# Kernel optimization log

Measured on AMD Instinct MI355X. Metric: run time of the kernel, lower is better.

Reference implementation:

```python
import jax, jax.numpy as jnp
import numpy as np

B, L, D, K, J = 8, 2048, 1024, 32, 512


def setup_inputs() -> dict:
    key = jax.random.key(0)
    ks = jax.random.split(key, 12)
    w = lambda k: jax.random.normal(k, (D, D), jnp.float32) * 0.02
    z = jnp.zeros((D,), jnp.float32)
    return {
        "seg0": jax.random.normal(ks[0], (B, L, D), jnp.float32),
        "seg1": jax.random.normal(ks[1], (B, L, D), jnp.float32),
        "prompt_embed": jax.random.normal(ks[2], (1, 1, D), jnp.float32),
        "Wq_mem": w(ks[3]), "bq_mem": z,
        "Wk_mem": w(ks[4]), "bk_mem": z,
        "Wq": w(ks[5]), "bq": z,
        "Wk": w(ks[6]), "bk": z,
        "Wv": w(ks[7]), "bv": z,
        "Wo": w(ks[8]), "bo": z,
    }


def reference(seg0, seg1, prompt_embed, Wq_mem, bq_mem, Wk_mem, bk_mem,
              Wq, bq, Wk, bk, Wv, bv, Wo, bo):
    scale = 1.0 / np.sqrt(D).astype(np.float32)  # n_heads=1 so d_k = d_model

    def backbone(X):  # single-head SDPA, X: [B, S, D]
        Q = X @ Wq + bq
        Kh = X @ Wk + bk
        V = X @ Wv + bv
        scores = jnp.einsum('bqd,bkd->bqk', Q, Kh) * scale
        attn = jax.nn.softmax(scores, axis=-1)
        out = jnp.einsum('bqk,bkd->bqd', attn, V)
        return out @ Wo + bo

    def summarize(H):  # -> [B, 1, D]
        T = jnp.broadcast_to(prompt_embed, (H.shape[0], 1, D))
        inp = jnp.concatenate([T, H[:, :J, :], T], axis=1)  # [B, J+2, D]
        return backbone(inp)[:, J:J + 1, :]

    # ---- segment 1: memory bank empty -> retrieval is zeros ----
    P0 = jnp.zeros((B, 1, D), seg0.dtype)
    input_h0 = jnp.concatenate([P0, seg0, P0], axis=1)  # [B, L+2, D]
    H_out0 = backbone(input_h0)[:, K + 1:L + K + 2, :]   # clamped slice -> [B, 2017, D]
    out0 = H_out0[:, :-1, :]                             # [B, 2016, D]
    M1 = H_out0[:, -1, :]                                # [B, D] stored memory
    prev_sensory = seg0[:, -K:, :]                       # [B, K, D]

    # ---- segment 2: soft retrieval over 1-entry memory bank ----
    S1 = summarize(seg1)                                 # [B, 1, D]
    M_past = M1[None]                                    # [1, B, D]
    Qn = S1 @ Wq_mem + bq_mem                            # [B, 1, D]
    Kp = M_past @ Wk_mem + bk_mem                        # [1, B, D]
    scores = jnp.matmul(Qn, jnp.swapaxes(Kp, -2, -1)) * scale  # [B, 1, B]
    attn = jax.nn.softmax(scores, axis=-1)
    P1 = jnp.matmul(attn, M_past)                        # [B, 1, D]

    input_h1 = jnp.concatenate([prev_sensory, P1, seg1, P1], axis=1)  # [B, K+L+2, D]
    H_out1 = backbone(input_h1)[:, K + 1:L + K + 2, :]   # [B, 2049, D]
    out1 = H_out1[:, :-1, :]                             # [B, 2048, D]
    return (out0, out1)
```

## Files before the change

kernel.cpp:

```cpp
#include <hip/hip_runtime.h>
#include <stdint.h>
#include <stddef.h>

#define DIM    1024
#define NBATCH 8
#define SEQL   2048
#define JSUM   512
#define SPMAX  2304
#define SPS    768

typedef unsigned long long ull;
typedef __attribute__((ext_vector_type(8))) __bf16 bf16x8;
typedef __attribute__((ext_vector_type(8))) short  short8;
typedef __attribute__((ext_vector_type(4))) float  floatx4;

__device__ __forceinline__ short f2bf(float f) {
  unsigned u = __builtin_bit_cast(unsigned, f);
  u = (u + 0x7fffu + ((u >> 16) & 1u)) >> 16;
  return (short)u;
}
__device__ __forceinline__ float bf2f(short s) {
  unsigned u = ((unsigned)(unsigned short)s) << 16;
  return __builtin_bit_cast(float, u);
}

__device__ __forceinline__ void glds16(const short* g, short8* l) {
  __builtin_amdgcn_global_load_lds(
      (const __attribute__((address_space(1))) unsigned int*)g,
      (__attribute__((address_space(3))) unsigned int*)l, 16, 0, 0);
}

#define VMCNT(n) do { asm volatile("s_waitcnt vmcnt(" #n ")" ::: "memory"); \
                      __builtin_amdgcn_sched_barrier(0); } while (0)

__device__ __forceinline__ void barrier_raw() {
  asm volatile("" ::: "memory");
  __builtin_amdgcn_s_barrier();
  asm volatile("" ::: "memory");
}

struct GemmP {
  const short* A; ull sA; int ldA;
  const short* B; ull sB; int ldB;
  short* C; ull sC;
  int N, Kd;
  const float* bias;
  float* dst0; int t_lo, t_hi, outT;
  float* dstSp; int t_sp, Spad;
  int gx;
  int nblk;
  int mode;
  int swiz;
};

__global__ __launch_bounds__(512, 2)
void gemm_nt(GemmP q0, GemmP q1)
{
  const int  pid = blockIdx.x;
  const bool s1  = pid >= q0.nblk;
  const GemmP& q = s1 ? q1 : q0;
  const int  lid = s1 ? (pid - q0.nblk) : pid;

  int tn, tm, bz;
  if (q.swiz == 1) {
    bz = lid & 7;
    const int s = lid >> 3;
    tn = s % q.gx;
    tm = s / q.gx;
  } else {
    tm = lid % q.gx;
    tn = lid / q.gx;
    bz = 0;
  }

  const short* A  = q.A + (ull)bz * q.sA;
  const short* Bm = q.B + (ull)bz * q.sB;

  const int tid  = threadIdx.x;
  const int wave = tid >> 6, lane = tid & 63;

  __shared__ short8 ldsA[2][2048];
  __shared__ short8 ldsB[2][2048];

  const int r0  = tid & 255;
  const int k80 = tid >> 8;
  const short* pA = A  + (long long)(tm * 256 + r0) * q.ldA + k80 * 8;
  const short* pB = Bm + (long long)(tn * 256 + r0) * q.ldB + k80 * 8;

  floatx4 acc[8][4];
#pragma unroll
  for (int i = 0; i < 8; i++)
#pragma unroll
    for (int j = 0; j < 4; j++) acc[i][j] = (floatx4)(0.0f);

  const int wm = (wave >> 2) * 128;
  const int wn = (wave & 3) * 64;
  const int fr = lane & 15;
  const int fq = lane >> 4;

  const int nt = q.Kd >> 6;

  glds16(pA,      &ldsA[0][tid]);
  glds16(pA + 16, &ldsA[0][tid + 512]);
  glds16(pB,      &ldsB[0][tid]);
  glds16(pB + 16, &ldsB[0][tid + 512]);
  glds16(pA + 32, &ldsA[0][1024 + tid]);
  glds16(pA + 48, &ldsA[0][1024 + tid + 512]);
  glds16(pB + 32, &ldsB[0][1024 + tid]);
  glds16(pB + 48, &ldsB[0][1024 + tid + 512]);
  VMCNT(4);
  barrier_raw();

  for (int t = 0; t < nt; t++) {
    const short8* LA = ldsA[t & 1];
    const short8* LB = ldsB[t & 1];
    const int  nb   = (t + 1) & 1;
    const int  koff = (t + 1) * 64;
    const bool stg  = (t + 1) < nt;

    bf16x8 af[4], bv[4];

    {
      const int ka = fq * 256;
#pragma unroll
      for (int n2 = 0; n2 < 4; n2++)
        bv[n2] = __builtin_bit_cast(bf16x8, LB[ka + wn + n2 * 16 + fr]);
#pragma unroll
      for (int mt = 0; mt < 4; mt++)
        af[mt] = __builtin_bit_cast(bf16x8, LA[ka + wm + mt * 16 + fr]);
      if (stg) {
        glds16(pA + koff,      &ldsA[nb][tid]);
        glds16(pA + koff + 16, &ldsA[nb][tid + 512]);
      }
      __builtin_amdgcn_s_setprio(1);
#pragma unroll
      for (int mt = 0; mt < 4; mt++)
#pragma unroll
        for (int n2 = 0; n2 < 4; n2++)
          acc[mt][n2] = __builtin_amdgcn_mfma_f32_16x16x32_bf16(
              af[mt], bv[n2], acc[mt][n2], 0, 0, 0);
      __builtin_amdgcn_s_setprio(0);
#pragma unroll
      for (int mt = 0; mt < 4; mt++)
        af[mt] = __builtin_bit_cast(bf16x8, LA[ka + wm + 64 + mt * 16 + fr]);
      if (stg) {
        glds16(pB + koff,      &ldsB[nb][tid]);
        glds16(pB + koff + 16, &ldsB[nb][tid + 512]);
      }
      __builtin_amdgcn_s_setprio(1);
#pragma unroll
      for (int mt = 0; mt < 4; mt++)
#pragma unroll
        for (int n2 = 0; n2 < 4; n2++)
          acc[4 + mt][n2] = __builtin_amdgcn_mfma_f32_16x16x32_bf16(
              af[mt], bv[n2], acc[4 + mt][n2], 0, 0, 0);
      __builtin_amdgcn_s_setprio(0);
      if (stg) VMCNT(4); else VMCNT(0);
      barrier_raw();
    }

    {
      const int ka = (fq + 4) * 256;
#pragma unroll
      for (int n2 = 0; n2 < 4; n2++)
        bv[n2] = __builtin_bit_cast(bf16x8, LB[ka + wn + n2 * 16 + fr]);
#pragma unroll
      for (int mt = 0; mt < 4; mt++)
        af[mt] = __builtin_bit_cast(bf16x8, LA[ka + wm + mt * 16 + fr]);
      if (stg) {
        glds16(pA + koff + 32, &ldsA[nb][1024 + tid]);
        glds16(pA + koff + 48, &ldsA[nb][1024 + tid + 512]);
      }
      __builtin_amdgcn_s_setprio(1);
#pragma unroll
      for (int mt = 0; mt < 4; mt++)
#pragma unroll
        for (int n2 = 0; n2 < 4; n2++)
          acc[mt][n2] = __builtin_amdgcn_mfma_f32_16x16x32_bf16(
              af[mt], bv[n2], acc[mt][n2], 0, 0, 0);
      __builtin_amdgcn_s_setprio(0);
#pragma unroll
      for (int mt = 0; mt < 4; mt++)
        af[mt] = __builtin_bit_cast(bf16x8, LA[ka + wm + 64 + mt * 16 + fr]);
      if (stg) {
        glds16(pB + koff + 32, &ldsB[nb][1024 + tid]);
        glds16(pB + koff + 48, &ldsB[nb][1024 + tid + 512]);
      }
      __builtin_amdgcn_s_setprio(1);
#pragma unroll
      for (int mt = 0; mt < 4; mt++)
#pragma unroll
        for (int n2 = 0; n2 < 4; n2++)
          acc[4 + mt][n2] = __builtin_amdgcn_mfma_f32_16x16x32_bf16(
              af[mt], bv[n2], acc[4 + mt][n2], 0, 0, 0);
      __builtin_amdgcn_s_setprio(0);
      if (stg) VMCNT(4);
      barrier_raw();
    }
  }

  if (q.mode == 3) {
    const int bb  = (tm * 256) / q.Spad;
    const int rb0 = tm * 256 - bb * q.Spad + wm + fq * 4;
#pragma unroll
    for (int mf = 0; mf < 8; mf++) {
#pragma unroll
      for (int n2 = 0; n2 < 4; n2++) {
        const int col = tn * 256 + wn + n2 * 16 + fr;
#pragma unroll
        for (int r = 0; r < 4; r++) {
          const int tt = rb0 + (mf >> 2) * 64 + (mf & 3) * 16 + r;
          float v = acc[mf][n2][r] + q.bias[col];
          if (tt >= q.t_lo && tt < q.t_hi)
            q.dst0[((size_t)bb * q.outT + (tt - q.t_lo)) * DIM + col] = v;
          else if (tt == q.t_sp)
            q.dstSp[(size_t)bb * DIM + col] = v;
        }
      }
    }
  } else {
    short* C = q.C + (ull)bz * q.sC;
#pragma unroll
    for (int mf = 0; mf < 8; mf++) {
#pragma unroll
      for (int n2 = 0; n2 < 4; n2++) {
        const int col = tn * 256 + wn + n2 * 16 + fr;
        float bn = (q.mode == 1) ? q.bias[col] : 0.0f;
#pragma unroll
        for (int r = 0; r < 4; r++) {
          const int row = tm * 256 + wm + (mf >> 2) * 64 + (mf & 3) * 16 + fq * 4 + r;
          float v = acc[mf][n2][r] + bn;
          if (q.mode == 2) v += q.bias[row];
          C[(size_t)row * q.N + col] = f2bf(v);
        }
      }
    }
  }
}

__global__ __launch_bounds__(256)
void softmax_rows2(short* __restrict__ SA0, int Spad0, int S0, int nx0,
                   short* __restrict__ SA1, int Spad1, int S1, float scale)
{
  __shared__ float buf[SPMAX];
  __shared__ float red[8];
  int t = blockIdx.x;
  const int b = blockIdx.y;
  short* row; int Spad, S;
  if (t < nx0) { row = SA0 + ((size_t)b * Spad0 + t) * Spad0; Spad = Spad0; S = S0; }
  else { t -= nx0; row = SA1 + ((size_t)b * Spad1 + t) * Spad1; Spad = Spad1; S = S1; }
  const int tid = threadIdx.x;
  const int nv = S >> 3;

  float mx = -1e30f;
  for (int g = tid; g < nv; g += 256) {
    short8 v = ((const short8*)row)[g];
#pragma unroll
    for (int j = 0; j < 8; j++) {
      float f = bf2f(v[j]) * scale;
      buf[g * 8 + j] = f;
      mx = fmaxf(mx, f);
    }
  }
  for (int i = (nv << 3) + tid; i < S; i += 256) {
    float f = bf2f(row[i]) * scale;
    buf[i] = f;
    mx = fmaxf(mx, f);
  }
  for (int off = 32; off; off >>= 1) mx = fmaxf(mx, __shfl_down(mx, off, 64));
  if ((tid & 63) == 0) red[tid >> 6] = mx;
  __syncthreads();
  if (tid == 0) {
    float m = red[0];
    for (int w = 1; w < 4; w++) m = fmaxf(m, red[w]);
    red[0] = m;
  }
  __syncthreads();
  mx = red[0];

  float sum = 0.f;
  for (int i = tid; i < S; i += 256) {
    float e = __expf(buf[i] - mx);
    buf[i] = e;
    sum += e;
  }
  for (int off = 32; off; off >>= 1) sum += __shfl_down(sum, off, 64);
  if ((tid & 63) == 0) red[4 + (tid >> 6)] = sum;
  __syncthreads();
  if (tid == 0) red[4] = 1.0f / (red[4] + red[5] + red[6] + red[7]);
  __syncthreads();
  const float rinv = red[4];

  for (int g = tid; g < nv; g += 256) {
    short8 o;
#pragma unroll
    for (int j = 0; j < 8; j++) o[j] = f2bf(buf[g * 8 + j] * rinv);
    ((short8*)row)[g] = o;
  }
  for (int i = (nv << 3) + tid; i < S; i += 256) row[i] = f2bf(buf[i] * rinv);
  for (int i = S + tid; i < Spad; i += 256) row[i] = 0;
}

__global__ __launch_bounds__(256)
void wtrans(const float* __restrict__ W, short* __restrict__ WT)
{
  __shared__ float tile[32][33];
  const int bn = blockIdx.x * 32, bk = blockIdx.y * 32;
  const int tx = threadIdx.x & 31, ty = threadIdx.x >> 5;
#pragma unroll
  for (int j = 0; j < 4; j++)
    tile[ty + j * 8][tx] = W[(size_t)(bk + ty + j * 8) * DIM + bn + tx];
  __syncthreads();
#pragma unroll
  for (int j = 0; j < 4; j++)
    WT[(size_t)(bn + ty + j * 8) * DIM + bk + tx] = f2bf(tile[tx][ty + j * 8]);
}

__global__ __launch_bounds__(256)
void bcat(const float* __restrict__ a, const float* __restrict__ b,
          float* __restrict__ o)
{
  const int i = blockIdx.x * 256 + threadIdx.x;
  o[i] = (i < DIM) ? a[i] : b[i - DIM];
}

__global__ __launch_bounds__(256)
void assemble0(const float* __restrict__ seg0, short* __restrict__ X)
{
  const int Spad = SPMAX;
  const int b = blockIdx.y;
  const size_t lin = ((size_t)blockIdx.x * 256 + threadIdx.x) * 4;
  const int t = (int)(lin >> 10), d = (int)(lin & 1023);
  float4 v = make_float4(0.f, 0.f, 0.f, 0.f);
  if (t >= 1 && t <= SEQL)
    v = *(const float4*)(seg0 + ((size_t)b * SEQL + (t - 1)) * DIM + d);
  union { short s[4]; ull u; } o;
  o.s[0] = f2bf(v.x); o.s[1] = f2bf(v.y); o.s[2] = f2bf(v.z); o.s[3] = f2bf(v.w);
  *(ull*)(X + (size_t)b * Spad * DIM + lin) = o.u;
}

__global__ __launch_bounds__(256)
void assembleS(const float* __restrict__ seg1, const float* __restrict__ prompt,
               short* __restrict__ X)
{
  const int Spad = SPS;
  const int b = blockIdx.y;
  const size_t lin = ((size_t)blockIdx.x * 256 + threadIdx.x) * 4;
  const int t = (int)(lin >> 10), d = (int)(lin & 1023);
  float4 v = make_float4(0.f, 0.f, 0.f, 0.f);
  if (t == 0 || t == JSUM + 1)
    v = *(const float4*)(prompt + d);
  else if (t >= 1 && t <= JSUM)
    v = *(const float4*)(seg1 + ((size_t)b * SEQL + (t - 1)) * DIM + d);
  union { short s[4]; ull u; } o;
  o.s[0] = f2bf(v.x); o.s[1] = f2bf(v.y); o.s[2] = f2bf(v.z); o.s[3] = f2bf(v.w);
  *(ull*)(X + (size_t)b * Spad * DIM + lin) = o.u;
}

__global__ __launch_bounds__(256)
void assemble1(const float* __restrict__ seg0, const float* __restrict__ seg1,
               const float* __restrict__ P1, short* __restrict__ X)
{
  const int Spad = SPMAX;
  const int b = blockIdx.y;
  const size_t lin = ((size_t)blockIdx.x * 256 + threadIdx.x) * 4;
  const int t = (int)(lin >> 10), d = (int)(lin & 1023);
  float4 v = make_float4(0.f, 0.f, 0.f, 0.f);
  if (t < 32)
    v = *(const float4*)(seg0 + ((size_t)b * SEQL + (SEQL - 32 + t)) * DIM + d);
  else if (t == 32 || t == 2081)
    v = *(const float4*)(P1 + (size_t)b * DIM + d);
  else if (t >= 33 && t <= 2080)
    v = *(const float4*)(seg1 + ((size_t)b * SEQL + (t - 33)) * DIM + d);
  union { short s[4]; ull u; } o;
  o.s[0] = f2bf(v.x); o.s[1] = f2bf(v.y); o.s[2] = f2bf(v.z); o.s[3] = f2bf(v.w);
  *(ull*)(X + (size_t)b * Spad * DIM + lin) = o.u;
}

__global__ __launch_bounds__(256)
void mem_proj(const float* __restrict__ Sb, const float* __restrict__ M1,
              const float* __restrict__ Wq_mem, const float* __restrict__ bq_mem,
              const float* __restrict__ Wk_mem, const float* __restrict__ bk_mem,
              float* __restrict__ Qn, float* __restrict__ Kp)
{
  const int n = blockIdx.x * 256 + threadIdx.x;
  const int b = blockIdx.y;
  const int w = blockIdx.z;
  const float* x    = w ? M1 : Sb;
  const float* W    = w ? Wk_mem : Wq_mem;
  const float* bias = w ? bk_mem : bq_mem;
  float* o          = w ? Kp : Qn;
  const float* xr = x + (size_t)b * DIM;
  float s = bias[n];
  for (int k = 0; k < DIM; k++) s += xr[k] * W[(size_t)k * DIM + n];
  o[(size_t)b * DIM + n] = s;
}

__global__ __launch_bounds__(256)
void mem_attn(const float* __restrict__ Qn, const float* __restrict__ Kp,
              const float* __restrict__ M1, float* __restrict__ P1, float scale)
{
  __shared__ float red[256];
  __shared__ float w8[8];
  const int b = blockIdx.x, tid = threadIdx.x;
  for (int bp = 0; bp < NBATCH; bp++) {
    float p = 0.f;
    for (int k = tid; k < DIM; k += 256)
      p += Qn[(size_t)b * DIM + k] * Kp[(size_t)bp * DIM + k];
    red[tid] = p; __syncthreads();
    for (int off = 128; off; off >>= 1) {
      if (tid < off) red[tid] += red[tid + off];
      __syncthreads();
    }
    if (tid == 0) w8[bp] = red[0] * scale;
    __syncthreads();
  }
  if (tid == 0) {
    float m = w8[0];
    for (int i = 1; i < NBATCH; i++) m = fmaxf(m, w8[i]);
    float s = 0.f;
    for (int i = 0; i < NBATCH; i++) { w8[i] = __expf(w8[i] - m); s += w8[i]; }
    for (int i = 0; i < NBATCH; i++) w8[i] /= s;
  }
  __syncthreads();
  for (int d = tid; d < DIM; d += 256) {
    float a = 0.f;
    for (int bp = 0; bp < NBATCH; bp++) a += w8[bp] * M1[(size_t)bp * DIM + d];
    P1[(size_t)b * DIM + d] = a;
  }
}

extern "C" void kernel_launch(void* const* d_in, const int* in_sizes, int n_in,
                              void* d_out, int out_size, void* d_ws, size_t ws_size,
                              hipStream_t stream)
{
  const float* seg0   = (const float*)d_in[0];
  const float* seg1   = (const float*)d_in[1];
  const float* prompt = (const float*)d_in[2];
  const float* Wq_mem = (const float*)d_in[3];
  const float* bq_mem = (const float*)d_in[4];
  const float* Wk_mem = (const float*)d_in[5];
  const float* bk_mem = (const float*)d_in[6];
  const float* Wq     = (const float*)d_in[7];
  const float* bq     = (const float*)d_in[8];
  const float* Wk     = (const float*)d_in[9];
  const float* bk     = (const float*)d_in[10];
  const float* Wv     = (const float*)d_in[11];
  const float* bv     = (const float*)d_in[12];
  const float* Wo     = (const float*)d_in[13];
  const float* bo     = (const float*)d_in[14];
  float* outp = (float*)d_out;

  const size_t WSZ   = (size_t)DIM * DIM * 2;
  const size_t XSZ   = (size_t)NBATCH * SPMAX * DIM * 2;
  const size_t SASZ  = (size_t)NBATCH * SPMAX * SPMAX * 2;
  const size_t XSZS  = (size_t)NBATCH * SPS * DIM * 2;
  const size_t SASZS = (size_t)NBATCH * SPS * SPS * 2;
  const size_t VSZ   = (size_t)NBATCH * DIM * 4;

  char* p = (char*)d_ws;
  short* WqT  = (short*)p; p += WSZ;
  short* WkT  = (short*)p; p += WSZ;
  short* WvT  = (short*)p; p += WSZ;
  short* WoT  = (short*)p; p += WSZ;
  short* X    = (short*)p; p += XSZ;
  short* QKb  = (short*)p; p += 2 * XSZ;
  short* Vt   = (short*)p; p += XSZ;
  short* Ctx  = (short*)p; p += XSZ;
  short* SA   = (short*)p; p += SASZ;
  short* XS   = (short*)p; p += XSZS;
  short* QKbS = (short*)p; p += 2 * XSZS;
  short* VtS  = (short*)p; p += XSZS;
  short* CtxS = (short*)p; p += XSZS;
  short* SAS  = (short*)p; p += SASZS;
  float* M1b  = (float*)p; p += VSZ;
  float* Sb   = (float*)p; p += VSZ;
  float* Qn   = (float*)p; p += VSZ;
  float* Kp   = (float*)p; p += VSZ;
  float* P1   = (float*)p; p += VSZ;
  float* bqk  = (float*)p; p += 2 * DIM * 4;

  const float scale = 0.03125f;
  dim3 blk(256, 1, 1);
  dim3 blkG(512, 1, 1);

  auto P = [](const short* A, ull sA, int ldA,
              const short* B, ull sB, int ldB,
              short* C, ull sC, int N, int Kd, const float* bias,
              float* dst0, int t_lo, int t_hi, int outT,
              float* dstSp, int t_sp, int Spad, int gx, int nblk,
              int mode, int swiz) {
    GemmP q{A, sA, ldA, B, sB, ldB, C, sC, N, Kd, bias,
            dst0, t_lo, t_hi, outT, dstSp, t_sp, Spad, gx, nblk, mode, swiz};
    return q;
  };

  wtrans<<<dim3(32, 32), blk, 0, stream>>>(Wq, WqT);
  wtrans<<<dim3(32, 32), blk, 0, stream>>>(Wk, WkT);
  wtrans<<<dim3(32, 32), blk, 0, stream>>>(Wv, WvT);
  wtrans<<<dim3(32, 32), blk, 0, stream>>>(Wo, WoT);
  bcat<<<dim3(8), blk, 0, stream>>>(bq, bk, bqk);

  assemble0<<<dim3(SPMAX, NBATCH), blk, 0, stream>>>(seg0, X);
  assembleS<<<dim3(SPS, NBATCH), blk, 0, stream>>>(seg1, prompt, XS);

  {
    GemmP a = P(X, 0, DIM, WqT, 0, DIM, QKb, 0, 2048, DIM, bqk,
                nullptr, 0, 0, 0, nullptr, -1, SPMAX, NBATCH * SPMAX / 256, 576, 1, 2);
    GemmP b = P(XS, 0, DIM, WqT, 0, DIM, QKbS, 0, 2048, DIM, bqk,
                nullptr, 0, 0, 0, nullptr, -1, SPS, NBATCH * SPS / 256, 192, 1, 2);
    gemm_nt<<<dim3(768), blkG, 0, stream>>>(a, b);
  }
  {
    GemmP a = P(WvT, 0, DIM, X, (ull)SPMAX * DIM, DIM,
                Vt, (ull)DIM * SPMAX, SPMAX, DIM, bv,
                nullptr, 0, 0, 0, nullptr, -1, SPMAX, SPMAX / 256, 288, 2, 1);
    GemmP b = P(WvT, 0, DIM, XS, (ull)SPS * DIM, DIM,
                VtS, (ull)DIM * SPS, SPS, DIM, bv,
                nullptr, 0, 0, 0, nullptr, -1, SPS, SPS / 256, 96, 2, 1);
    gemm_nt<<<dim3(384), blkG, 0, stream>>>(a, b);
  }
  {
    GemmP a = P(QKb, (ull)SPMAX * 2048, 2048, QKb + DIM, (ull)SPMAX * 2048, 2048,
                SA, (ull)SPMAX * SPMAX, SPMAX, DIM, nullptr,
                nullptr, 0, 0, 0, nullptr, -1, SPMAX, SPMAX / 256, 648, 0, 1);
    GemmP b = P(QKbS, (ull)SPS * 2048, 2048, QKbS + DIM, (ull)SPS * 2048, 2048,
                SAS, (ull)SPS * SPS, SPS, DIM, nullptr,
                nullptr, 0, 0, 0, nullptr, -1, SPS, SPS / 256, 72, 0, 1);
    gemm_nt<<<dim3(720), blkG, 0, stream>>>(a, b);
  }
  softmax_rows2<<<dim3(SPMAX + SPS, NBATCH), blk, 0, stream>>>(
      SA, SPMAX, 2050, SPMAX, SAS, SPS, 514, scale);
  {
    GemmP a = P(SA, (ull)SPMAX * SPMAX, SPMAX, Vt, (ull)DIM * SPMAX, SPMAX,
                Ctx, (ull)SPMAX * DIM, DIM, 2112, nullptr,
                nullptr, 0, 0, 0, nullptr, -1, SPMAX, DIM / 256, 288, 0, 1);
    GemmP b = P(SAS, (ull)SPS * SPS, SPS, VtS, (ull)DIM * SPS, SPS,
                CtxS, (ull)SPS * DIM, DIM, 576, nullptr,
                nullptr, 0, 0, 0, nullptr, -1, SPS, DIM / 256, 96, 0, 1);
    gemm_nt<<<dim3(384), blkG, 0, stream>>>(a, b);
  }
  {
    GemmP a = P(Ctx, 0, DIM, WoT, 0, DIM, nullptr, 0, DIM, DIM, bo,
                outp, 33, 2049, 2016, M1b, 2049, SPMAX, NBATCH * SPMAX / 256, 288, 3, 2);
    GemmP b = P(CtxS, 0, DIM, WoT, 0, DIM, nullptr, 0, DIM, DIM, bo,
                nullptr, 0, 0, 0, Sb, JSUM, SPS, NBATCH * SPS / 256, 96, 3, 2);
    gemm_nt<<<dim3(384), blkG, 0, stream>>>(a, b);
  }

  mem_proj<<<dim3(DIM / 256, NBATCH, 2), blk, 0, stream>>>(
      Sb, M1b, Wq_mem, bq_mem, Wk_mem, bk_mem, Qn, Kp);
  mem_attn<<<dim3(NBATCH), blk, 0, stream>>>(Qn, Kp, M1b, P1, scale);

  assemble1<<<dim3(SPMAX, NBATCH), blk, 0, stream>>>(seg0, seg1, P1, X);
  {
    GemmP a = P(X, 0, DIM, WqT, 0, DIM, QKb, 0, 2048, DIM, bqk,
                nullptr, 0, 0, 0, nullptr, -1, SPMAX, NBATCH * SPMAX / 256, 576, 1, 2);
    GemmP b = P(WvT, 0, DIM, X, (ull)SPMAX * DIM, DIM,
                Vt, (ull)DIM * SPMAX, SPMAX, DIM, bv,
                nullptr, 0, 0, 0, nullptr, -1, SPMAX, SPMAX / 256, 288, 2, 1);
    gemm_nt<<<dim3(864), blkG, 0, stream>>>(a, b);
  }
  {
    GemmP a = P(QKb, (ull)SPMAX * 2048, 2048, QKb + DIM, (ull)SPMAX * 2048, 2048,
                SA, (ull)SPMAX * SPMAX, SPMAX, DIM, nullptr,
                nullptr, 0, 0, 0, nullptr, -1, SPMAX, SPMAX / 256, 648, 0, 1);
    gemm_nt<<<dim3(648), blkG, 0, stream>>>(a, a);
  }
  softmax_rows2<<<dim3(SPMAX, NBATCH), blk, 0, stream>>>(
      SA, SPMAX, 2082, SPMAX, SA, SPMAX, 2082, scale);
  {
    GemmP a = P(SA, (ull)SPMAX * SPMAX, SPMAX, Vt, (ull)DIM * SPMAX, SPMAX,
                Ctx, (ull)SPMAX * DIM, DIM, 2112, nullptr,
                nullptr, 0, 0, 0, nullptr, -1, SPMAX, DIM / 256, 288, 0, 1);
    gemm_nt<<<dim3(288), blkG, 0, stream>>>(a, a);
  }
  {
    GemmP a = P(Ctx, 0, DIM, WoT, 0, DIM, nullptr, 0, DIM, DIM, bo,
                outp + (size_t)NBATCH * 2016 * DIM, 33, 2081, 2048,
                nullptr, -1, SPMAX, NBATCH * SPMAX / 256, 288, 3, 2);
    gemm_nt<<<dim3(288), blkG, 0, stream>>>(a, a);
  }
}
```

Baseline: 1.484 ms.

## Use 1024-thread GEMM blocks with 64x64 per-wave subtiles and unfuse QK/V launch

The bf16 GEMM block grows from 512 to 1024 threads (16 waves). Each wave now computes a 64x64 subtile instead of 128x64, halving accumulator registers, and each thread issues half as many global-to-LDS loads per stage. An extra barrier is added before each MFMA phase. The segment-2 fused QK-projection and V-transpose GEMM launch is split into two separate launches. The intent is more waves per CU for latency hiding, at the cost of lower per-wave arithmetic intensity, more LDS traffic per MFMA and extra synchronisation.

After: 1.990 ms. 1.34x slower.

```diff
diff --git a/kernel.cpp b/kernel.cpp
--- a/kernel.cpp
+++ b/kernel.cpp
@@ -53,7 +53,7 @@
   int swiz;
 };
 
-__global__ __launch_bounds__(512, 2)
+__global__ __launch_bounds__(1024)
 void gemm_nt(GemmP q0, GemmP q1)
 {
   const int  pid = blockIdx.x;
@@ -87,13 +87,13 @@
   const short* pA = A  + (long long)(tm * 256 + r0) * q.ldA + k80 * 8;
   const short* pB = Bm + (long long)(tn * 256 + r0) * q.ldB + k80 * 8;
 
-  floatx4 acc[8][4];
-#pragma unroll
-  for (int i = 0; i < 8; i++)
+  floatx4 acc[4][4];
+#pragma unroll
+  for (int i = 0; i < 4; i++)
 #pragma unroll
     for (int j = 0; j < 4; j++) acc[i][j] = (floatx4)(0.0f);
 
-  const int wm = (wave >> 2) * 128;
+  const int wm = (wave >> 2) * 64;
   const int wn = (wave & 3) * 64;
   const int fr = lane & 15;
   const int fq = lane >> 4;
@@ -101,14 +101,10 @@
   const int nt = q.Kd >> 6;
 
   glds16(pA,      &ldsA[0][tid]);
-  glds16(pA + 16, &ldsA[0][tid + 512]);
   glds16(pB,      &ldsB[0][tid]);
-  glds16(pB + 16, &ldsB[0][tid + 512]);
   glds16(pA + 32, &ldsA[0][1024 + tid]);
-  glds16(pA + 48, &ldsA[0][1024 + tid + 512]);
   glds16(pB + 32, &ldsB[0][1024 + tid]);
-  glds16(pB + 48, &ldsB[0][1024 + tid + 512]);
-  VMCNT(4);
+  VMCNT(2);
   barrier_raw();
 
   for (int t = 0; t < nt; t++) {
@@ -123,15 +119,16 @@
     {
       const int ka = fq * 256;
 #pragma unroll
+      for (int mt = 0; mt < 4; mt++)
+        af[mt] = __builtin_bit_cast(bf16x8, LA[ka + wm + mt * 16 + fr]);
+#pragma unroll
       for (int n2 = 0; n2 < 4; n2++)
         bv[n2] = __builtin_bit_cast(bf16x8, LB[ka + wn + n2 * 16 + fr]);
-#pragma unroll
-      for (int mt = 0; mt < 4; mt++)
-        af[mt] = __builtin_bit_cast(bf16x8, LA[ka + wm + mt * 16 + fr]);
       if (stg) {
-        glds16(pA + koff,      &ldsA[nb][tid]);
-        glds16(pA + koff + 16, &ldsA[nb][tid + 512]);
+        glds16(pA + koff, &ldsA[nb][tid]);
+        glds16(pB + koff, &ldsB[nb][tid]);
       }
+      barrier_raw();
       __builtin_amdgcn_s_setprio(1);
 #pragma unroll
       for (int mt = 0; mt < 4; mt++)
@@ -140,37 +137,23 @@
           acc[mt][n2] = __builtin_amdgcn_mfma_f32_16x16x32_bf16(
               af[mt], bv[n2], acc[mt][n2], 0, 0, 0);
       __builtin_amdgcn_s_setprio(0);
-#pragma unroll
-      for (int mt = 0; mt < 4; mt++)
-        af[mt] = __builtin_bit_cast(bf16x8, LA[ka + wm + 64 + mt * 16 + fr]);
-      if (stg) {
-        glds16(pB + koff,      &ldsB[nb][tid]);
-        glds16(pB + koff + 16, &ldsB[nb][tid + 512]);
-      }
-      __builtin_amdgcn_s_setprio(1);
-#pragma unroll
-      for (int mt = 0; mt < 4; mt++)
-#pragma unroll
-        for (int n2 = 0; n2 < 4; n2++)
-          acc[4 + mt][n2] = __builtin_amdgcn_mfma_f32_16x16x32_bf16(
-              af[mt], bv[n2], acc[4 + mt][n2], 0, 0, 0);
-      __builtin_amdgcn_s_setprio(0);
-      if (stg) VMCNT(4); else VMCNT(0);
+      if (stg) VMCNT(2); else VMCNT(0);
       barrier_raw();
     }
 
     {
       const int ka = (fq + 4) * 256;
 #pragma unroll
+      for (int mt = 0; mt < 4; mt++)
+        af[mt] = __builtin_bit_cast(bf16x8, LA[ka + wm + mt * 16 + fr]);
+#pragma unroll
       for (int n2 = 0; n2 < 4; n2++)
         bv[n2] = __builtin_bit_cast(bf16x8, LB[ka + wn + n2 * 16 + fr]);
-#pragma unroll
-      for (int mt = 0; mt < 4; mt++)
-        af[mt] = __builtin_bit_cast(bf16x8, LA[ka + wm + mt * 16 + fr]);
       if (stg) {
         glds16(pA + koff + 32, &ldsA[nb][1024 + tid]);
-        glds16(pA + koff + 48, &ldsA[nb][1024 + tid + 512]);
+        glds16(pB + koff + 32, &ldsB[nb][1024 + tid]);
       }
+      barrier_raw();
       __builtin_amdgcn_s_setprio(1);
 #pragma unroll
       for (int mt = 0; mt < 4; mt++)
@@ -179,22 +162,7 @@
           acc[mt][n2] = __builtin_amdgcn_mfma_f32_16x16x32_bf16(
               af[mt], bv[n2], acc[mt][n2], 0, 0, 0);
       __builtin_amdgcn_s_setprio(0);
-#pragma unroll
-      for (int mt = 0; mt < 4; mt++)
-        af[mt] = __builtin_bit_cast(bf16x8, LA[ka + wm + 64 + mt * 16 + fr]);
-      if (stg) {
-        glds16(pB + koff + 32, &ldsB[nb][1024 + tid]);
-        glds16(pB + koff + 48, &ldsB[nb][1024 + tid + 512]);
-      }
-      __builtin_amdgcn_s_setprio(1);
-#pragma unroll
-      for (int mt = 0; mt < 4; mt++)
-#pragma unroll
-        for (int n2 = 0; n2 < 4; n2++)
-          acc[4 + mt][n2] = __builtin_amdgcn_mfma_f32_16x16x32_bf16(
-              af[mt], bv[n2], acc[4 + mt][n2], 0, 0, 0);
-      __builtin_amdgcn_s_setprio(0);
-      if (stg) VMCNT(4);
+      if (stg) VMCNT(2);
       barrier_raw();
     }
   }
@@ -203,13 +171,13 @@
     const int bb  = (tm * 256) / q.Spad;
     const int rb0 = tm * 256 - bb * q.Spad + wm + fq * 4;
 #pragma unroll
-    for (int mf = 0; mf < 8; mf++) {
+    for (int mf = 0; mf < 4; mf++) {
 #pragma unroll
       for (int n2 = 0; n2 < 4; n2++) {
         const int col = tn * 256 + wn + n2 * 16 + fr;
 #pragma unroll
         for (int r = 0; r < 4; r++) {
-          const int tt = rb0 + (mf >> 2) * 64 + (mf & 3) * 16 + r;
+          const int tt = rb0 + mf * 16 + r;
           float v = acc[mf][n2][r] + q.bias[col];
           if (tt >= q.t_lo && tt < q.t_hi)
             q.dst0[((size_t)bb * q.outT + (tt - q.t_lo)) * DIM + col] = v;
@@ -221,14 +189,14 @@
   } else {
     short* C = q.C + (ull)bz * q.sC;
 #pragma unroll
-    for (int mf = 0; mf < 8; mf++) {
+    for (int mf = 0; mf < 4; mf++) {
 #pragma unroll
       for (int n2 = 0; n2 < 4; n2++) {
         const int col = tn * 256 + wn + n2 * 16 + fr;
         float bn = (q.mode == 1) ? q.bias[col] : 0.0f;
 #pragma unroll
         for (int r = 0; r < 4; r++) {
-          const int row = tm * 256 + wm + (mf >> 2) * 64 + (mf & 3) * 16 + fq * 4 + r;
+          const int row = tm * 256 + wm + mf * 16 + fq * 4 + r;
           float v = acc[mf][n2][r] + bn;
           if (q.mode == 2) v += q.bias[row];
           C[(size_t)row * q.N + col] = f2bf(v);
@@ -482,7 +450,7 @@
 
   const float scale = 0.03125f;
   dim3 blk(256, 1, 1);
-  dim3 blkG(512, 1, 1);
+  dim3 blkG(1024, 1, 1);
 
   auto P = [](const short* A, ull sA, int ldA,
               const short* B, ull sB, int ldB,
@@ -556,10 +524,13 @@
   {
     GemmP a = P(X, 0, DIM, WqT, 0, DIM, QKb, 0, 2048, DIM, bqk,
                 nullptr, 0, 0, 0, nullptr, -1, SPMAX, NBATCH * SPMAX / 256, 576, 1, 2);
-    GemmP b = P(WvT, 0, DIM, X, (ull)SPMAX * DIM, DIM,
+    gemm_nt<<<dim3(576), blkG, 0, stream>>>(a, a);
+  }
+  {
+    GemmP a = P(WvT, 0, DIM, X, (ull)SPMAX * DIM, DIM,
                 Vt, (ull)DIM * SPMAX, SPMAX, DIM, bv,
                 nullptr, 0, 0, 0, nullptr, -1, SPMAX, SPMAX / 256, 288, 2, 1);
-    gemm_nt<<<dim3(864), blkG, 0, stream>>>(a, b);
+    gemm_nt<<<dim3(288), blkG, 0, stream>>>(a, a);
   }
   {
     GemmP a = P(QKb, (ull)SPMAX * 2048, 2048, QKb + DIM, (ull)SPMAX * 2048, 2048,
```
